# Optimization experiments

Measured on AMD Instinct MI355X. Metric: run time of the kernel, lower is better.

## Reference

```python
import jax, jax.numpy as jnp
import numpy as np

VOCAB, IMG_EMB, EMB, HID, P = 10000, 1024, 512, 512, 49
B, T = 64, 50


def setup_inputs() -> dict:
    key = jax.random.key(0)
    ks = jax.random.split(key, 16)
    def lin(k, fin, fout):
        k1, k2 = jax.random.split(k)
        s = 1.0 / np.sqrt(fin)
        return (jax.random.uniform(k1, (fin, fout), minval=-s, maxval=s),
                jax.random.uniform(k2, (fout,), minval=-s, maxval=s))
    Wv, bv = lin(ks[0], IMG_EMB, EMB)
    Wh, bh = lin(ks[1], EMB, HID)
    Wm, bm = lin(ks[2], EMB, HID)
    Wl, bl = lin(ks[3], 2 * EMB + HID, 5 * HID)  # LSTM fc on cat([w_t, vg, h])
    Wav, bav = lin(ks[4], HID, HID)
    Wah, bah = lin(ks[5], HID, HID)
    Was, bas = lin(ks[6], HID, HID)
    Waz, baz = lin(ks[7], HID, 1)
    Wp, bp = lin(ks[8], HID, VOCAB)
    emb = jax.random.normal(ks[9], (VOCAB, EMB)) * 0.02
    return {
        'v': jax.random.normal(ks[10], (B, P, IMG_EMB)),
        'w': jax.random.randint(ks[11], (B, T), 0, VOCAB),
        'lengths': jax.random.randint(ks[12], (B,), 0, T),
        'emb': emb,
        'Wv': Wv, 'bv': bv, 'Wh': Wh, 'bh': bh, 'Wm': Wm, 'bm': bm,
        'Wl': Wl, 'bl': bl,
        'Wav': Wav, 'bav': bav, 'Wah': Wah, 'bah': bah,
        'Was': Was, 'bas': bas, 'Waz': Waz, 'baz': baz,
        'Wp': Wp, 'bp': bp,
    }


def reference(v, w, lengths, emb, Wv, bv, Wh, bh, Wm, bm, Wl, bl,
              Wav, bav, Wah, bah, Was, bas, Waz, baz, Wp, bp):
    we = emb[w]                        # [B,T,E] word embeddings
    v = v @ Wv + bv                    # [B,P,E] projected visual features
    vg = v.mean(axis=1)                # [B,E] global visual feature
    h0 = vg @ Wh + bh                  # [B,H]
    m0 = vg @ Wm + bm                  # [B,H]
    pv = v @ Wav + bav                 # precompute attention proj of v [B,P,H]

    def step(carry, wt):
        h_, m_ = carry
        x = jnp.concatenate([wt, vg, h_], axis=-1)        # [B, 2E+H]
        i, f, o, g, m5 = jnp.split(x @ Wl + bl, 5, axis=-1)
        i = jax.nn.sigmoid(i)
        f = jax.nn.sigmoid(f)
        o = jax.nn.sigmoid(o)
        m = i * jnp.tanh(m5) + f * m_
        tm = jnp.tanh(m)
        h = o * tm
        s = g * tm                                        # sentinel gate
        # adaptive attention over P regions + sentinel h slot
        ph = (h @ Wah + bah)[:, None, :]                  # [B,1,H]
        ps = (s @ Was + bas)[:, None, :]                  # [B,1,H]
        z = jnp.tanh(jnp.concatenate([pv, ph], axis=1) + ps)  # [B,P+1,H]
        a = jax.nn.softmax(z @ Waz + baz, axis=1)         # [B,P+1,1]
        c = jnp.sum(a * jnp.concatenate([v, h[:, None, :]], axis=1), axis=1)
        p = jax.nn.softmax((c + h) @ Wp + bp, axis=-1)    # [B,V]
        return (h, m), p

    _, ps = jax.lax.scan(step, (h0, m0), jnp.swapaxes(we, 0, 1))
    ps = jnp.swapaxes(ps, 0, 1)                           # [B,T,V]
    mask = jnp.arange(ps.shape[1])[None, :] < lengths[:, None]
    return ps * mask[..., None].astype(ps.dtype)
```

## Files before the change

kernel.cpp:

```cpp
#include <hip/hip_runtime.h>
#include <hip/hip_bf16.h>
#include <cstdint>
#include <cstddef>

#define Bn 64
#define Tn 50
#define Pn 49
#define En 512
#define Hn 512
#define Vn 10000
#define IEn 1024
#define G5 2560

typedef __attribute__((ext_vector_type(8))) short bf16x8;
typedef __attribute__((ext_vector_type(4))) float f32x4;

__device__ __forceinline__ float sigm(float x)  { return 1.0f / (1.0f + __expf(-x)); }
__device__ __forceinline__ float tanh_f(float x){ return 1.0f - 2.0f / (1.0f + __expf(2.0f * x)); }

__device__ __forceinline__ unsigned short f2b(float f) {
    union { float f; unsigned int u; } c; c.f = f;
    unsigned int u = c.u;
    u += 0x7fffu + ((u >> 16) & 1u);
    return (unsigned short)(u >> 16);
}
__device__ __forceinline__ float b2f(unsigned short u) {
    union { unsigned int u; float f; } c; c.u = ((unsigned int)u) << 16;
    return c.f;
}

template<bool GATHER>
__global__ __launch_bounds__(256)
void gemm64(const float* __restrict__ A, int lda,
            const float* __restrict__ B,
            float* __restrict__ C,
            int M, int N, int K,
            const float* __restrict__ bias,
            const float* __restrict__ rowadd, int rowDiv, long rowStride,
            const int* __restrict__ gidx)
{
    const int n0 = blockIdx.x * 64;
    const int m0 = blockIdx.y * 64;
    const long koff = (long)blockIdx.z * K;
    const float* Bp = B + koff * N;
    float* Cp = C + (gridDim.z > 1 ? (size_t)blockIdx.z * (size_t)M * (size_t)N : (size_t)0);

    __shared__ float As[16][64];
    __shared__ float Bs[16][64];

    const int tid = threadIdx.x;
    const int tx = tid & 15;
    const int ty = tid >> 4;
    const int ra = tid >> 2;
    const int ca = (tid & 3) << 2;

    long arow = GATHER ? (long)gidx[m0 + ra] : (long)(m0 + ra);
    const float* Arow = A + arow * (long)lda + koff + ca;

    const int kl = ty;
    const int nb = tx << 2;
    const int ncol = n0 + nb;

    float acc[4][4] = {{0.f,0.f,0.f,0.f},{0.f,0.f,0.f,0.f},{0.f,0.f,0.f,0.f},{0.f,0.f,0.f,0.f}};

    for (int k0 = 0; k0 < K; k0 += 16) {
        float4 av = *(const float4*)(Arow + k0);
        float4 bv;
        const float* bptr = Bp + (long)(k0 + kl) * N + ncol;
        if (ncol + 3 < N) {
            bv = *(const float4*)bptr;
        } else {
            bv.x = (ncol + 0 < N) ? bptr[0] : 0.f;
            bv.y = (ncol + 1 < N) ? bptr[1] : 0.f;
            bv.z = (ncol + 2 < N) ? bptr[2] : 0.f;
            bv.w = (ncol + 3 < N) ? bptr[3] : 0.f;
        }
        __syncthreads();
        As[ca + 0][ra] = av.x; As[ca + 1][ra] = av.y;
        As[ca + 2][ra] = av.z; As[ca + 3][ra] = av.w;
        *(float4*)&Bs[kl][nb] = bv;
        __syncthreads();
        #pragma unroll
        for (int kk = 0; kk < 16; kk++) {
            const float4 a = *(const float4*)&As[kk][ty << 2];
            const float4 b = *(const float4*)&Bs[kk][tx << 2];
            const float a_[4] = {a.x, a.y, a.z, a.w};
            const float b_[4] = {b.x, b.y, b.z, b.w};
            #pragma unroll
            for (int i = 0; i < 4; i++)
                #pragma unroll
                for (int j = 0; j < 4; j++)
                    acc[i][j] = fmaf(a_[i], b_[j], acc[i][j]);
        }
    }

    #pragma unroll
    for (int i = 0; i < 4; i++) {
        const int rr = m0 + (ty << 2) + i;
        #pragma unroll
        for (int j = 0; j < 4; j++) {
            const int cc = n0 + (tx << 2) + j;
            if (cc < N) {
                float v = acc[i][j];
                if (bias)   v += bias[cc];
                if (rowadd) v += rowadd[(long)(rr / rowDiv) * rowStride + cc];
                Cp[(long)rr * N + cc] = v;
            }
        }
    }
}

template<int OUTF, int OUTB, int GM, int SWZ>
__global__ __launch_bounds__(256)
void gemm_mfma(const unsigned short* __restrict__ A,
               const unsigned short* __restrict__ BT,
               float* __restrict__ Cf, unsigned short* __restrict__ Cb,
               int M, int N, int K,
               const float* __restrict__ bias,
               const float* __restrict__ rowadd, int rowDiv,
               const int* __restrict__ ridx, const int* __restrict__ dcnt,
               int mtiles)
{
    __shared__ __align__(16) unsigned short Asm[128][40];
    __shared__ __align__(16) unsigned short Bsm[128][40];

    int Meff = M;
    if (GM) Meff = *dcnt;
    int m0, n0;
    if (SWZ) {
        const int nwg = gridDim.x;
        const int q = nwg >> 3, rm = nwg & 7;
        const int xcd = blockIdx.x & 7, pos = blockIdx.x >> 3;
        const int swz = (xcd < rm ? xcd * (q + 1) : rm * (q + 1) + (xcd - rm) * q) + pos;
        m0 = (swz % mtiles) * 128;
        n0 = (swz / mtiles) * 128;
    } else {
        n0 = blockIdx.x * 128;
        m0 = blockIdx.y * 128;
    }
    if (GM && m0 >= Meff) return;

    const int tid = threadIdx.x;
    const int lane = tid & 63;
    const int wid = tid >> 6;
    const int wm = wid >> 1;
    const int wn = wid & 1;

    const int r0 = tid >> 2;
    const int kg = tid & 3;

    const int ar0 = m0 + r0, ar1 = m0 + r0 + 64;
    const int br0 = n0 + r0, br1 = n0 + r0 + 64;
    long arow0, arow1;
    if (GM) {
        arow0 = (ar0 < Meff) ? (long)ridx[ar0] : 0;
        arow1 = (ar1 < Meff) ? (long)ridx[ar1] : 0;
    } else {
        arow0 = ar0; arow1 = ar1;
    }

    f32x4 acc[4][4] = {};
    const uint4 zero4 = {0u, 0u, 0u, 0u};

    uint4 a0, a1, b0, b1;
    {
        const long ka = (long)kg * 8;
        a0 = (GM || ar0 < Meff) ? *(const uint4*)(A + arow0 * K + ka) : zero4;
        a1 = (GM || ar1 < Meff) ? *(const uint4*)(A + arow1 * K + ka) : zero4;
        b0 = (br0 < N) ? *(const uint4*)(BT + (long)br0 * K + ka) : zero4;
        b1 = (br1 < N) ? *(const uint4*)(BT + (long)br1 * K + ka) : zero4;
    }

    for (int k0 = 0; k0 < K; k0 += 32) {
        __syncthreads();
        *(uint4*)&Asm[r0     ][kg * 8] = a0;
        *(uint4*)&Asm[r0 + 64][kg * 8] = a1;
        *(uint4*)&Bsm[r0     ][kg * 8] = b0;
        *(uint4*)&Bsm[r0 + 64][kg * 8] = b1;
        __syncthreads();

        if (k0 + 32 < K) {
            const long ka = (long)(k0 + 32) + kg * 8;
            a0 = (GM || ar0 < Meff) ? *(const uint4*)(A + arow0 * K + ka) : zero4;
            a1 = (GM || ar1 < Meff) ? *(const uint4*)(A + arow1 * K + ka) : zero4;
            b0 = (br0 < N) ? *(const uint4*)(BT + (long)br0 * K + ka) : zero4;
            b1 = (br1 < N) ? *(const uint4*)(BT + (long)br1 * K + ka) : zero4;
        }

        bf16x8 af[4], bfr[4];
        const int arow = wm * 64 + (lane & 15);
        const int brow = wn * 64 + (lane & 15);
        const int kcol = (lane >> 4) * 8;
        #pragma unroll
        for (int i = 0; i < 4; i++) {
            af[i]  = *(const bf16x8*)&Asm[arow + i * 16][kcol];
            bfr[i] = *(const bf16x8*)&Bsm[brow + i * 16][kcol];
        }
        #pragma unroll
        for (int mi = 0; mi < 4; mi++)
            #pragma unroll
            for (int ni = 0; ni < 4; ni++)
                acc[mi][ni] = __builtin_amdgcn_mfma_f32_16x16x32_bf16(af[mi], bfr[ni], acc[mi][ni], 0, 0, 0);
    }

    const int crow = m0 + wm * 64 + (lane >> 4) * 4;
    const int ccol0 = n0 + wn * 64 + (lane & 15);
    #pragma unroll
    for (int ni = 0; ni < 4; ni++) {
        const int col = ccol0 + ni * 16;
        if (col >= N) continue;
        const float bvv = bias ? bias[col] : 0.f;
        #pragma unroll
        for (int mi = 0; mi < 4; mi++) {
            #pragma unroll
            for (int r = 0; r < 4; r++) {
                const int rr = crow + mi * 16 + r;
                if (rr < Meff) {
                    const long orow = GM ? (long)ridx[rr] : (long)rr;
                    float v = acc[mi][ni][r] + bvv;
                    if (rowadd) v += rowadd[(long)(rr / rowDiv) * N + col];
                    if (OUTF) Cf[orow * N + col] = v;
                    if (OUTB) Cb[orow * N + col] = f2b(v);
                }
            }
        }
    }
}

__global__ __launch_bounds__(256)
void transpose_bf16(const float* __restrict__ in, unsigned short* __restrict__ out,
                    int K, int N, int istride)
{
    __shared__ float tile[32][33];
    const int k0 = blockIdx.y * 32;
    const int n0 = blockIdx.x * 32;
    const int tx = threadIdx.x & 31, ty = threadIdx.x >> 5;
    #pragma unroll
    for (int j = 0; j < 4; j++) {
        int k = k0 + ty + j * 8, n = n0 + tx;
        tile[ty + j * 8][tx] = (k < K && n < N) ? in[(long)k * istride + n] : 0.f;
    }
    __syncthreads();
    #pragma unroll
    for (int j = 0; j < 4; j++) {
        int n = n0 + ty + j * 8, k = k0 + tx;
        if (n < N && k < K) out[(long)n * K + k] = f2b(tile[tx][ty + j * 8]);
    }
}

__global__ __launch_bounds__(256)
void transpose2_G5(const float* __restrict__ Wl,
                   unsigned short* __restrict__ O0, unsigned short* __restrict__ O1)
{
    const float* in = Wl + (blockIdx.z ? (size_t)1024 * G5 : (size_t)0);
    unsigned short* out = blockIdx.z ? O1 : O0;
    __shared__ float tile[32][33];
    const int k0 = blockIdx.y * 32;
    const int n0 = blockIdx.x * 32;
    const int tx = threadIdx.x & 31, ty = threadIdx.x >> 5;
    #pragma unroll
    for (int j = 0; j < 4; j++)
        tile[ty + j * 8][tx] = in[(long)(k0 + ty + j * 8) * G5 + n0 + tx];
    __syncthreads();
    #pragma unroll
    for (int j = 0; j < 4; j++)
        out[(long)(n0 + ty + j * 8) * 512 + k0 + tx] = f2b(tile[tx][ty + j * 8]);
}

__global__ __launch_bounds__(256)
void transpose3_bf16(const float* __restrict__ A0, const float* __restrict__ A1,
                     const float* __restrict__ A2,
                     unsigned short* __restrict__ O0, unsigned short* __restrict__ O1,
                     unsigned short* __restrict__ O2)
{
    const float* in = (blockIdx.z == 0) ? A0 : (blockIdx.z == 1) ? A1 : A2;
    unsigned short* out = (blockIdx.z == 0) ? O0 : (blockIdx.z == 1) ? O1 : O2;
    __shared__ float tile[32][33];
    const int k0 = blockIdx.y * 32;
    const int n0 = blockIdx.x * 32;
    const int tx = threadIdx.x & 31, ty = threadIdx.x >> 5;
    #pragma unroll
    for (int j = 0; j < 4; j++)
        tile[ty + j * 8][tx] = in[(long)(k0 + ty + j * 8) * 512 + n0 + tx];
    __syncthreads();
    #pragma unroll
    for (int j = 0; j < 4; j++)
        out[(long)(n0 + ty + j * 8) * 512 + k0 + tx] = f2b(tile[tx][ty + j * 8]);
}

__global__ void convert_bf16(const float* __restrict__ in, unsigned short* __restrict__ out, int n4)
{
    int i = blockIdx.x * 256 + threadIdx.x;
    if (i < n4) {
        float4 v = ((const float4*)in)[i];
        ushort4 u;
        u.x = f2b(v.x); u.y = f2b(v.y); u.z = f2b(v.z); u.w = f2b(v.w);
        ((ushort4*)out)[i] = u;
    }
}

__global__ void gather_convert(const float* __restrict__ emb, const int* __restrict__ w,
                               unsigned short* __restrict__ out)
{
    const int r = blockIdx.x;
    const long row = w[r];
    const float4 v = ((const float4*)(emb + row * 512))[threadIdx.x];
    ushort4 u;
    u.x = f2b(v.x); u.y = f2b(v.y); u.z = f2b(v.z); u.w = f2b(v.w);
    ((ushort4*)(out + (long)r * 512))[threadIdx.x] = u;
}

__global__ void compact_rows(const int* __restrict__ len, int* __restrict__ ridx, int* __restrict__ dcnt)
{
    const int b = threadIdx.x;
    int L = len[b]; L = L < 0 ? 0 : (L > Tn ? Tn : L);
    int off = L;
    #pragma unroll
    for (int s = 1; s < 64; s <<= 1) {
        int n = __shfl_up(off, s);
        if (b >= s) off += n;
    }
    const int start = off - L;
    if (b == 63) *dcnt = off;
    for (int t = 0; t < L; t++) ridx[start + t] = b * Tn + t;
}

__global__ void vg_mean(const unsigned short* __restrict__ vproj, float* __restrict__ vg)
{
    const int tid = blockIdx.x * 256 + threadIdx.x;
    const int b = tid >> 9, e = tid & 511;
    const unsigned short* p = vproj + (long)b * Pn * En + e;
    float s = 0.f;
    #pragma unroll 7
    for (int q = 0; q < Pn; q++) s += b2f(p[q * En]);
    vg[tid] = s * (1.0f / 49.0f);
}

__global__ void h0m0(const float* __restrict__ vg,
                     const float* __restrict__ Wh, const float* __restrict__ bh,
                     const float* __restrict__ Wm, const float* __restrict__ bm,
                     unsigned short* __restrict__ h0b, float* __restrict__ m)
{
    __shared__ float vgs[512];
    const int b = blockIdx.x, e = threadIdx.x;
    vgs[e] = vg[b * 512 + e];
    __syncthreads();
    float a1 = bh[e], a2 = bm[e];
    #pragma unroll 8
    for (int k = 0; k < 512; k++) {
        const float x = vgs[k];
        a1 = fmaf(x, Wh[(long)k * 512 + e], a1);
        a2 = fmaf(x, Wm[(long)k * 512 + e], a2);
    }
    h0b[b * 512 + e] = f2b(a1);
    m[b * 512 + e] = a2;
}

__global__ __launch_bounds__(256)
void scan_step(int t, const float* __restrict__ base,
               const unsigned short* __restrict__ hcur,
               unsigned short* __restrict__ hnxt,
               float* __restrict__ mF,
               const unsigned short* __restrict__ W3T,
               float* __restrict__ HsF, unsigned short* __restrict__ Hsb,
               unsigned short* __restrict__ Ssb)
{
    __shared__ __align__(16) unsigned short Wh_s[5][8][520];

    const int tid = threadIdx.x;
    const int lane = tid & 63, wv = tid >> 6;
    const int e0 = blockIdx.x * 8;
    const int col = lane & 15;
    const int fk = (lane >> 4) * 8;
    const int bb = wv * 16 + (lane & 15);

    bf16x8 Ah[16];
    #pragma unroll
    for (int ch = 0; ch < 16; ch++)
        Ah[ch] = *(const bf16x8*)(hcur + (long)bb * 512 + ch * 32 + fk);

    for (int idx = tid; idx < 40 * 64; idx += 256) {
        const int row = idx >> 6, seg = idx & 63;
        const int g = row >> 3, c = row & 7;
        *(uint4*)&Wh_s[g][c][seg * 8] =
            *(const uint4*)(W3T + (long)(g * 512 + e0 + c) * 512 + seg * 8);
    }

    const int rbase = wv * 16 + (lane >> 4) * 4;
    const int ecol = e0 + (col & 7);
    float bse[5][4], mv[4];
    if (col < 8) {
        #pragma unroll
        for (int r = 0; r < 4; r++) {
            const long rrow = (long)(rbase + r) * Tn + t;
            const float* bp = base + rrow * G5 + ecol;
            bse[0][r] = bp[0];    bse[1][r] = bp[512];  bse[2][r] = bp[1024];
            bse[3][r] = bp[1536]; bse[4][r] = bp[2048];
            mv[r] = mF[(rbase + r) * 512 + ecol];
        }
    }

    __syncthreads();

    const unsigned short* B0 = &Wh_s[(col >> 3)    ][col & 7][0];
    const unsigned short* B1 = &Wh_s[2 + (col >> 3)][col & 7][0];
    const unsigned short* B2 = &Wh_s[4][col & 7][0];

    f32x4 a0 = {}, a1 = {}, a2 = {};
    #pragma unroll
    for (int ch = 0; ch < 16; ch++) {
        const int ko = ch * 32 + fk;
        a0 = __builtin_amdgcn_mfma_f32_16x16x32_bf16(Ah[ch], *(const bf16x8*)(B0 + ko), a0, 0, 0, 0);
        a1 = __builtin_amdgcn_mfma_f32_16x16x32_bf16(Ah[ch], *(const bf16x8*)(B1 + ko), a1, 0, 0, 0);
        a2 = __builtin_amdgcn_mfma_f32_16x16x32_bf16(Ah[ch], *(const bf16x8*)(B2 + ko), a2, 0, 0, 0);
    }

    #pragma unroll
    for (int r = 0; r < 4; r++) {
        const float fsh = __shfl_xor(a0[r], 8);
        const float gsh = __shfl_xor(a1[r], 8);
        if (col < 8) {
            const int b = rbase + r;
            const float gi = a0[r] + bse[0][r];
            const float gf = fsh   + bse[1][r];
            const float go = a1[r] + bse[2][r];
            const float gg = gsh   + bse[3][r];
            const float g5 = a2[r] + bse[4][r];
            const float iv = sigm(gi), fv = sigm(gf), ov = sigm(go);
            const float mn = fmaf(iv, tanh_f(g5), fv * mv[r]);
            const float tm = tanh_f(mn);
            const float hh = ov * tm, ss = gg * tm;
            const unsigned short hhi = f2b(hh);
            const long hoff = (long)b * 512 + ecol;
            const long rrow = (long)b * Tn + t;
            mF[hoff] = mn;
            hnxt[hoff] = hhi;
            HsF[rrow * 512 + ecol] = hh;
            Hsb[rrow * 512 + ecol] = hhi;
            Ssb[rrow * 512 + ecol] = f2b(ss);
        }
    }
}

__global__ __launch_bounds__(256)
void attn(const unsigned short* __restrict__ vproj, const float* __restrict__ pv,
          const float* __restrict__ PH, const float* __restrict__ PS,
          const float* __restrict__ Hs, const float* __restrict__ Waz,
          const float* __restrict__ baz, unsigned short* __restrict__ CHb,
          const int* __restrict__ len)
{
    const int r = (blockIdx.x & 7) * 400 + (blockIdx.x >> 3);
    const int b = r / Tn;
    if ((r % Tn) >= len[b]) return;
    const int tid = threadIdx.x;
    const int lane = tid & 63, wid = tid >> 6;

    __shared__ float ps_s[512];
    __shared__ float ph_s[512];
    __shared__ float alog[64];

    for (int i = tid; i < 512; i += 256) {
        ps_s[i] = PS[(long)r * 512 + i];
        ph_s[i] = PH[(long)r * 512 + i];
    }
    __syncthreads();

    const float4 wz0 = *(const float4*)(Waz + lane * 8);
    const float4 wz1 = *(const float4*)(Waz + lane * 8 + 4);
    const float4 q0  = *(const float4*)&ps_s[lane * 8];
    const float4 q1  = *(const float4*)&ps_s[lane * 8 + 4];

    for (int slot = wid; slot < Pn + 1; slot += 4) {
        const float* src = (slot < Pn) ? (pv + ((long)b * Pn + slot) * 512)
                                       : (const float*)ph_s;
        const float4 x0 = *(const float4*)(src + lane * 8);
        const float4 x1 = *(const float4*)(src + lane * 8 + 4);
        float d = 0.f;
        d = fmaf(tanh_f(x0.x + q0.x), wz0.x, d);
        d = fmaf(tanh_f(x0.y + q0.y), wz0.y, d);
        d = fmaf(tanh_f(x0.z + q0.z), wz0.z, d);
        d = fmaf(tanh_f(x0.w + q0.w), wz0.w, d);
        d = fmaf(tanh_f(x1.x + q1.x), wz1.x, d);
        d = fmaf(tanh_f(x1.y + q1.y), wz1.y, d);
        d = fmaf(tanh_f(x1.z + q1.z), wz1.z, d);
        d = fmaf(tanh_f(x1.w + q1.w), wz1.w, d);
        #pragma unroll
        for (int s = 32; s >= 1; s >>= 1) d += __shfl_xor(d, s);
        if (lane == 0) alog[slot] = d + baz[0];
    }
    __syncthreads();

    if (wid == 0) {
        const float v = (lane < Pn + 1) ? alog[lane] : -3.4e38f;
        float mx = v;
        #pragma unroll
        for (int s = 32; s >= 1; s >>= 1) mx = fmaxf(mx, __shfl_xor(mx, s));
        const float ev = (lane < Pn + 1) ? __expf(v - mx) : 0.f;
        float sm = ev;
        #pragma unroll
        for (int s = 32; s >= 1; s >>= 1) sm += __shfl_xor(sm, s);
        if (lane < Pn + 1) alog[lane] = ev / sm;
    }
    __syncthreads();

    const float a49 = alog[Pn];
    for (int ee = tid; ee < 512; ee += 256) {
        const float hval = Hs[(long)r * 512 + ee];
        float c = a49 * hval;
        const unsigned short* vp = vproj + (long)b * Pn * 512 + ee;
        #pragma unroll 7
        for (int q = 0; q < Pn; q++) c = fmaf(alog[q], b2f(vp[q * 512]), c);
        CHb[(long)r * 512 + ee] = f2b(c + hval);
    }
}

__global__ __launch_bounds__(256)
void softmax_mask(float* __restrict__ out, const int* __restrict__ lengths)
{
    const int r = blockIdx.x, b = r / Tn, t = r % Tn;
    float* row = out + (long)r * Vn;
    const int tid = threadIdx.x;
    float4* row4 = (float4*)row;

    if (t >= lengths[b]) {
        f32x4* rowv = (f32x4*)row;
        const f32x4 z = {0.f, 0.f, 0.f, 0.f};
        for (int i = tid; i < Vn / 4; i += 256)
            __builtin_nontemporal_store(z, &rowv[i]);
        return;
    }

    __shared__ float red[4];
    const int lane = tid & 63, wid = tid >> 6;

    float4 rv[10];
    float mx = -3.4e38f;
    #pragma unroll
    for (int j = 0; j < 10; j++) {
        const int i = tid + j * 256;
        if (i < Vn / 4) {
            rv[j] = row4[i];
            mx = fmaxf(mx, fmaxf(fmaxf(rv[j].x, rv[j].y), fmaxf(rv[j].z, rv[j].w)));
        }
    }
    #pragma unroll
    for (int s = 32; s >= 1; s >>= 1) mx = fmaxf(mx, __shfl_xor(mx, s));
    if (lane == 0) red[wid] = mx;
    __syncthreads();
    mx = fmaxf(fmaxf(red[0], red[1]), fmaxf(red[2], red[3]));
    __syncthreads();

    float sm = 0.f;
    #pragma unroll
    for (int j = 0; j < 10; j++) {
        const int i = tid + j * 256;
        if (i < Vn / 4) {
            rv[j].x = __expf(rv[j].x - mx);
            rv[j].y = __expf(rv[j].y - mx);
            rv[j].z = __expf(rv[j].z - mx);
            rv[j].w = __expf(rv[j].w - mx);
            sm += rv[j].x + rv[j].y + rv[j].z + rv[j].w;
        }
    }
    #pragma unroll
    for (int s = 32; s >= 1; s >>= 1) sm += __shfl_xor(sm, s);
    if (lane == 0) red[wid] = sm;
    __syncthreads();
    sm = red[0] + red[1] + red[2] + red[3];
    const float inv = 1.0f / sm;

    #pragma unroll
    for (int j = 0; j < 10; j++) {
        const int i = tid + j * 256;
        if (i < Vn / 4) {
            rv[j].x *= inv; rv[j].y *= inv; rv[j].z *= inv; rv[j].w *= inv;
            row4[i] = rv[j];
        }
    }
}

extern "C" void kernel_launch(void* const* d_in, const int* in_sizes, int n_in,
                              void* d_out, int out_size, void* d_ws, size_t ws_size,
                              hipStream_t stream)
{
    (void)in_sizes; (void)n_in; (void)out_size; (void)ws_size;
    const float* v   = (const float*)d_in[0];
    const int*   w   = (const int*)  d_in[1];
    const int*   len = (const int*)  d_in[2];
    const float* emb = (const float*)d_in[3];
    const float* Wv  = (const float*)d_in[4];
    const float* bv  = (const float*)d_in[5];
    const float* Wh  = (const float*)d_in[6];
    const float* bh  = (const float*)d_in[7];
    const float* Wm  = (const float*)d_in[8];
    const float* bm  = (const float*)d_in[9];
    const float* Wl  = (const float*)d_in[10];
    const float* bl  = (const float*)d_in[11];
    const float* Wav = (const float*)d_in[12];
    const float* bav = (const float*)d_in[13];
    const float* Wah = (const float*)d_in[14];
    const float* bah = (const float*)d_in[15];
    const float* Was = (const float*)d_in[16];
    const float* bas = (const float*)d_in[17];
    const float* Waz = (const float*)d_in[18];
    const float* baz = (const float*)d_in[19];
    const float* Wp  = (const float*)d_in[20];
    const float* bp  = (const float*)d_in[21];
    float* out_f = (float*)d_out;

    char* wsp = (char*)d_ws;
    size_t off = 0;
    auto walloc = [&](size_t bytes) -> void* {
        void* r = wsp + off;
        off += (bytes + 255) & ~(size_t)255;
        return r;
    };
    unsigned short* WpT    = (unsigned short*)walloc((size_t)Vn * 512 * 2);
    unsigned short* WvT    = (unsigned short*)walloc((size_t)512 * 1024 * 2);
    unsigned short* WlT0   = (unsigned short*)walloc((size_t)G5 * 512 * 2);
    unsigned short* WavT   = (unsigned short*)walloc((size_t)512 * 512 * 2);
    unsigned short* WahT   = (unsigned short*)walloc((size_t)512 * 512 * 2);
    unsigned short* WasT   = (unsigned short*)walloc((size_t)512 * 512 * 2);
    unsigned short* vprojb = (unsigned short*)walloc((size_t)3136 * 512 * 2);
    unsigned short* CHb    = (unsigned short*)walloc((size_t)3200 * 512 * 2);
    float* vg   = (float*)walloc((size_t)64 * 512 * 4);
    unsigned short* hB = (unsigned short*)walloc((size_t)2 * 64 * 512 * 2);
    float* mbuf = (float*)walloc((size_t)64 * 512 * 4);
    float* vgw  = (float*)walloc((size_t)64 * G5 * 4);
    int*   ridx = (int*)walloc((size_t)3200 * 4);
    int*   dcnt = (int*)walloc(256);

    char* sp = (char*)(out_f + (size_t)3200 * G5);
    size_t off2 = 0;
    auto salloc = [&](size_t bytes) -> void* {
        void* r = sp + off2;
        off2 += (bytes + 255) & ~(size_t)255;
        return r;
    };
    unsigned short* vB  = (unsigned short*)salloc((size_t)3136 * 1024 * 2);
    unsigned short* WEb = (unsigned short*)salloc((size_t)3200 * 512 * 2);
    float* pvb = (float*)salloc((size_t)3136 * 512 * 4);
    float* HsF = (float*)salloc((size_t)3200 * 512 * 4);
    unsigned short* Hsb = (unsigned short*)salloc((size_t)3200 * 512 * 2);
    unsigned short* Ssb = (unsigned short*)salloc((size_t)3200 * 512 * 2);
    float* PHb = (float*)salloc((size_t)3200 * 512 * 4);
    float* PSb = (float*)salloc((size_t)3200 * 512 * 4);
    unsigned short* W3T = (unsigned short*)salloc((size_t)G5 * 512 * 2);

    transpose_bf16<<<dim3(512/32, 1024/32), 256, 0, stream>>>(Wv, WvT, 1024, 512, 512);
    transpose2_G5<<<dim3(G5/32, 16, 2), 256, 0, stream>>>(Wl, WlT0, W3T);
    transpose3_bf16<<<dim3(16, 16, 3), 256, 0, stream>>>(Wav, Wah, Was, WavT, WahT, WasT);
    transpose_bf16<<<dim3((Vn + 31)/32, 16), 256, 0, stream>>>(Wp, WpT, 512, Vn, Vn);
    convert_bf16<<<(3136*1024/4 + 255)/256, 256, 0, stream>>>(v, vB, 3136*1024/4);
    gather_convert<<<3200, 128, 0, stream>>>(emb, w, WEb);
    compact_rows<<<1, 64, 0, stream>>>(len, ridx, dcnt);

    gemm_mfma<0,1,0,0><<<dim3(4, 25), 256, 0, stream>>>(vB, WvT, nullptr, vprojb,
                                                        3136, 512, 1024, bv, nullptr, 1,
                                                        nullptr, nullptr, 0);
    vg_mean<<<128, 256, 0, stream>>>(vprojb, vg);
    h0m0<<<64, 512, 0, stream>>>(vg, Wh, bh, Wm, bm, hB, mbuf);
    gemm64<false><<<dim3(40, 1, 1), 256, 0, stream>>>(vg, 512, Wl + (size_t)512 * G5, vgw,
                                                      64, G5, 512, bl, nullptr, 1, 0, nullptr);
    gemm_mfma<1,0,0,0><<<dim3(4, 25), 256, 0, stream>>>(vprojb, WavT, pvb, nullptr,
                                                        3136, 512, 512, bav, nullptr, 1,
                                                        nullptr, nullptr, 0);
    gemm_mfma<1,0,0,1><<<500, 256, 0, stream>>>(WEb, WlT0, out_f, nullptr,
                                                3200, G5, 512, nullptr, vgw, Tn,
                                                nullptr, nullptr, 25);
    for (int t = 0; t < Tn; t++) {
        const size_t cur = (size_t)(t & 1) * (64 * 512);
        const size_t nxt = (size_t)((t + 1) & 1) * (64 * 512);
        scan_step<<<64, 256, 0, stream>>>(t, out_f, hB + cur, hB + nxt, mbuf, W3T,
                                          HsF, Hsb, Ssb);
    }
    gemm_mfma<1,0,1,0><<<dim3(4, 25), 256, 0, stream>>>(Hsb, WahT, PHb, nullptr,
                                                        3200, 512, 512, bah, nullptr, 1,
                                                        ridx, dcnt, 0);
    gemm_mfma<1,0,1,0><<<dim3(4, 25), 256, 0, stream>>>(Ssb, WasT, PSb, nullptr,
                                                        3200, 512, 512, bas, nullptr, 1,
                                                        ridx, dcnt, 0);
    attn<<<3200, 256, 0, stream>>>(vprojb, pvb, PHb, PSb, HsF, Waz, baz, CHb, len);
    gemm_mfma<1,0,1,1><<<1975, 256, 0, stream>>>(CHb, WpT, out_f, nullptr,
                                                 3200, Vn, 512, bp, nullptr, 1,
                                                 ridx, dcnt, 25);
    softmax_mask<<<3200, 256, 0, stream>>>(out_f, len);
}
```

Baseline: 802.5 us.

## Fuse attention projections into scan steps, compact LSTM input GEMM, add wide output GEMM

Removes the two separate Wah/Was projection GEMMs. Each scan step now also computes the previous step's h·Wah and s·Was from the h it already holds in registers, with one extra step launched at the end. The word-embedding LSTM input GEMM now computes only the valid (compacted) rows, and its rowadd indexing uses the real output row. The vocabulary projection uses a new 128x256-tile GEMM to cut the number of workgroups and reuse A tiles more. The trade-offs are one extra scan launch, more shared memory per scan block, and higher register pressure in the wide GEMM.

```diff
diff --git a/kernel.cpp b/kernel.cpp
--- a/kernel.cpp
+++ b/kernel.cpp
@@ -218,9 +218,109 @@
                 if (rr < Meff) {
                     const long orow = GM ? (long)ridx[rr] : (long)rr;
                     float v = acc[mi][ni][r] + bvv;
-                    if (rowadd) v += rowadd[(long)(rr / rowDiv) * N + col];
+                    if (rowadd) v += rowadd[(orow / rowDiv) * N + col];
                     if (OUTF) Cf[orow * N + col] = v;
                     if (OUTB) Cb[orow * N + col] = f2b(v);
+                }
+            }
+        }
+    }
+}
+
+__global__ __launch_bounds__(256)
+void gemm_n256(const unsigned short* __restrict__ A,
+               const unsigned short* __restrict__ BT,
+               float* __restrict__ Cf,
+               int N, int K,
+               const float* __restrict__ bias,
+               const int* __restrict__ ridx, const int* __restrict__ dcnt,
+               int mtiles)
+{
+    __shared__ __align__(16) unsigned short Asm[128][40];
+    __shared__ __align__(16) unsigned short Bsm[256][40];
+
+    const int Meff = *dcnt;
+    int m0, n0;
+    {
+        const int nwg = gridDim.x;
+        const int q = nwg >> 3, rm = nwg & 7;
+        const int xcd = blockIdx.x & 7, pos = blockIdx.x >> 3;
+        const int swz = (xcd < rm ? xcd * (q + 1) : rm * (q + 1) + (xcd - rm) * q) + pos;
+        m0 = (swz % mtiles) * 128;
+        n0 = (swz / mtiles) * 256;
+    }
+    if (m0 >= Meff) return;
+
+    const int tid = threadIdx.x;
+    const int lane = tid & 63;
+    const int wid = tid >> 6;
+    const int wm = wid >> 1;
+    const int wn = wid & 1;
+    const int r0 = tid >> 2;
+    const int kg = tid & 3;
+
+    const int ar0 = m0 + r0, ar1 = m0 + r0 + 64;
+    const long arow0 = (ar0 < Meff) ? (long)ridx[ar0] : 0;
+    const long arow1 = (ar1 < Meff) ? (long)ridx[ar1] : 0;
+
+    f32x4 acc[4][8] = {};
+    const uint4 zero4 = {0u, 0u, 0u, 0u};
+
+    uint4 aR0, aR1, bR[4];
+    auto load = [&](int k0) {
+        const long ka = (long)k0 + kg * 8;
+        aR0 = *(const uint4*)(A + arow0 * K + ka);
+        aR1 = *(const uint4*)(A + arow1 * K + ka);
+        #pragma unroll
+        for (int j = 0; j < 4; j++) {
+            const int br = n0 + r0 + j * 64;
+            bR[j] = (br < N) ? *(const uint4*)(BT + (long)br * K + ka) : zero4;
+        }
+    };
+    load(0);
+
+    const int arowf = wm * 64 + (lane & 15);
+    const int browf = wn * 128 + (lane & 15);
+    const int kcol = (lane >> 4) * 8;
+
+    for (int k0 = 0; k0 < K; k0 += 32) {
+        __syncthreads();
+        *(uint4*)&Asm[r0     ][kg * 8] = aR0;
+        *(uint4*)&Asm[r0 + 64][kg * 8] = aR1;
+        #pragma unroll
+        for (int j = 0; j < 4; j++)
+            *(uint4*)&Bsm[r0 + j * 64][kg * 8] = bR[j];
+        __syncthreads();
+
+        if (k0 + 32 < K) load(k0 + 32);
+
+        bf16x8 af[4], bfr[8];
+        #pragma unroll
+        for (int i = 0; i < 4; i++) af[i] = *(const bf16x8*)&Asm[arowf + i * 16][kcol];
+        #pragma unroll
+        for (int i = 0; i < 8; i++) bfr[i] = *(const bf16x8*)&Bsm[browf + i * 16][kcol];
+        #pragma unroll
+        for (int mi = 0; mi < 4; mi++)
+            #pragma unroll
+            for (int ni = 0; ni < 8; ni++)
+                acc[mi][ni] = __builtin_amdgcn_mfma_f32_16x16x32_bf16(af[mi], bfr[ni], acc[mi][ni], 0, 0, 0);
+    }
+
+    const int crow = m0 + wm * 64 + (lane >> 4) * 4;
+    const int ccol0 = n0 + wn * 128 + (lane & 15);
+    #pragma unroll
+    for (int ni = 0; ni < 8; ni++) {
+        const int col = ccol0 + ni * 16;
+        if (col >= N) continue;
+        const float bvv = bias[col];
+        #pragma unroll
+        for (int mi = 0; mi < 4; mi++) {
+            #pragma unroll
+            for (int r = 0; r < 4; r++) {
+                const int rr = crow + mi * 16 + r;
+                if (rr < Meff) {
+                    const long orow = (long)ridx[rr];
+                    Cf[orow * N + col] = acc[mi][ni][r] + bvv;
                 }
             }
         }
@@ -362,10 +462,15 @@
                unsigned short* __restrict__ hnxt,
                float* __restrict__ mF,
                const unsigned short* __restrict__ W3T,
+               const unsigned short* __restrict__ WahT,
+               const unsigned short* __restrict__ WasT,
+               const float* __restrict__ bah, const float* __restrict__ bas,
                float* __restrict__ HsF, unsigned short* __restrict__ Hsb,
-               unsigned short* __restrict__ Ssb)
+               unsigned short* __restrict__ Ssb,
+               float* __restrict__ PHb, float* __restrict__ PSb)
 {
     __shared__ __align__(16) unsigned short Wh_s[5][8][520];
+    __shared__ __align__(16) unsigned short B3_s[16][520];
 
     const int tid = threadIdx.x;
     const int lane = tid & 63, wv = tid >> 6;
@@ -385,11 +490,18 @@
         *(uint4*)&Wh_s[g][c][seg * 8] =
             *(const uint4*)(W3T + (long)(g * 512 + e0 + c) * 512 + seg * 8);
     }
+    for (int idx = tid; idx < 16 * 64; idx += 256) {
+        const int row = idx >> 6, seg = idx & 63;
+        const unsigned short* src = (row < 8)
+            ? WahT + (long)(e0 + row) * 512
+            : WasT + (long)(e0 + row - 8) * 512;
+        *(uint4*)&B3_s[row][seg * 8] = *(const uint4*)(src + seg * 8);
+    }
 
     const int rbase = wv * 16 + (lane >> 4) * 4;
     const int ecol = e0 + (col & 7);
     float bse[5][4], mv[4];
-    if (col < 8) {
+    if (t < Tn && col < 8) {
         #pragma unroll
         for (int r = 0; r < 4; r++) {
             const long rrow = (long)(rbase + r) * Tn + t;
@@ -402,42 +514,57 @@
 
     __syncthreads();
 
-    const unsigned short* B0 = &Wh_s[(col >> 3)    ][col & 7][0];
-    const unsigned short* B1 = &Wh_s[2 + (col >> 3)][col & 7][0];
-    const unsigned short* B2 = &Wh_s[4][col & 7][0];
-
-    f32x4 a0 = {}, a1 = {}, a2 = {};
-    #pragma unroll
-    for (int ch = 0; ch < 16; ch++) {
-        const int ko = ch * 32 + fk;
-        a0 = __builtin_amdgcn_mfma_f32_16x16x32_bf16(Ah[ch], *(const bf16x8*)(B0 + ko), a0, 0, 0, 0);
-        a1 = __builtin_amdgcn_mfma_f32_16x16x32_bf16(Ah[ch], *(const bf16x8*)(B1 + ko), a1, 0, 0, 0);
-        a2 = __builtin_amdgcn_mfma_f32_16x16x32_bf16(Ah[ch], *(const bf16x8*)(B2 + ko), a2, 0, 0, 0);
-    }
-
-    #pragma unroll
-    for (int r = 0; r < 4; r++) {
-        const float fsh = __shfl_xor(a0[r], 8);
-        const float gsh = __shfl_xor(a1[r], 8);
-        if (col < 8) {
-            const int b = rbase + r;
-            const float gi = a0[r] + bse[0][r];
-            const float gf = fsh   + bse[1][r];
-            const float go = a1[r] + bse[2][r];
-            const float gg = gsh   + bse[3][r];
-            const float g5 = a2[r] + bse[4][r];
-            const float iv = sigm(gi), fv = sigm(gf), ov = sigm(go);
-            const float mn = fmaf(iv, tanh_f(g5), fv * mv[r]);
-            const float tm = tanh_f(mn);
-            const float hh = ov * tm, ss = gg * tm;
-            const unsigned short hhi = f2b(hh);
-            const long hoff = (long)b * 512 + ecol;
-            const long rrow = (long)b * Tn + t;
-            mF[hoff] = mn;
-            hnxt[hoff] = hhi;
-            HsF[rrow * 512 + ecol] = hh;
-            Hsb[rrow * 512 + ecol] = hhi;
-            Ssb[rrow * 512 + ecol] = f2b(ss);
+    if (t > 0) {
+        const unsigned short* B3p = &B3_s[col][0];
+        f32x4 a3 = {};
+        #pragma unroll
+        for (int ch = 0; ch < 16; ch++)
+            a3 = __builtin_amdgcn_mfma_f32_16x16x32_bf16(Ah[ch], *(const bf16x8*)(B3p + ch * 32 + fk), a3, 0, 0, 0);
+        const float pb = (col < 8) ? bah[ecol] : bas[ecol];
+        float* dst = (col < 8) ? PHb : PSb;
+        #pragma unroll
+        for (int r = 0; r < 4; r++)
+            dst[((long)(rbase + r) * Tn + (t - 1)) * 512 + ecol] = a3[r] + pb;
+    }
+
+    if (t < Tn) {
+        const unsigned short* B0 = &Wh_s[(col >> 3)    ][col & 7][0];
+        const unsigned short* B1 = &Wh_s[2 + (col >> 3)][col & 7][0];
+        const unsigned short* B2 = &Wh_s[4][col & 7][0];
+
+        f32x4 a0 = {}, a1 = {}, a2 = {};
+        #pragma unroll
+        for (int ch = 0; ch < 16; ch++) {
+            const int ko = ch * 32 + fk;
+            a0 = __builtin_amdgcn_mfma_f32_16x16x32_bf16(Ah[ch], *(const bf16x8*)(B0 + ko), a0, 0, 0, 0);
+            a1 = __builtin_amdgcn_mfma_f32_16x16x32_bf16(Ah[ch], *(const bf16x8*)(B1 + ko), a1, 0, 0, 0);
+            a2 = __builtin_amdgcn_mfma_f32_16x16x32_bf16(Ah[ch], *(const bf16x8*)(B2 + ko), a2, 0, 0, 0);
+        }
+
+        #pragma unroll
+        for (int r = 0; r < 4; r++) {
+            const float fsh = __shfl_xor(a0[r], 8);
+            const float gsh = __shfl_xor(a1[r], 8);
+            if (col < 8) {
+                const int b = rbase + r;
+                const float gi = a0[r] + bse[0][r];
+                const float gf = fsh   + bse[1][r];
+                const float go = a1[r] + bse[2][r];
+                const float gg = gsh   + bse[3][r];
+                const float g5 = a2[r] + bse[4][r];
+                const float iv = sigm(gi), fv = sigm(gf), ov = sigm(go);
+                const float mn = fmaf(iv, tanh_f(g5), fv * mv[r]);
+                const float tm = tanh_f(mn);
+                const float hh = ov * tm, ss = gg * tm;
+                const unsigned short hhi = f2b(hh);
+                const long hoff = (long)b * 512 + ecol;
+                const long rrow = (long)b * Tn + t;
+                mF[hoff] = mn;
+                hnxt[hoff] = hhi;
+                HsF[rrow * 512 + ecol] = hh;
+                Hsb[rrow * 512 + ecol] = hhi;
+                Ssb[rrow * 512 + ecol] = f2b(ss);
+            }
         }
     }
 }
@@ -665,24 +792,17 @@
     gemm_mfma<1,0,0,0><<<dim3(4, 25), 256, 0, stream>>>(vprojb, WavT, pvb, nullptr,
                                                         3136, 512, 512, bav, nullptr, 1,
                                                         nullptr, nullptr, 0);
-    gemm_mfma<1,0,0,1><<<500, 256, 0, stream>>>(WEb, WlT0, out_f, nullptr,
+    gemm_mfma<1,0,1,1><<<500, 256, 0, stream>>>(WEb, WlT0, out_f, nullptr,
                                                 3200, G5, 512, nullptr, vgw, Tn,
-                                                nullptr, nullptr, 25);
-    for (int t = 0; t < Tn; t++) {
+                                                ridx, dcnt, 25);
+    for (int t = 0; t <= Tn; t++) {
         const size_t cur = (size_t)(t & 1) * (64 * 512);
         const size_t nxt = (size_t)((t + 1) & 1) * (64 * 512);
         scan_step<<<64, 256, 0, stream>>>(t, out_f, hB + cur, hB + nxt, mbuf, W3T,
-                                          HsF, Hsb, Ssb);
-    }
-    gemm_mfma<1,0,1,0><<<dim3(4, 25), 256, 0, stream>>>(Hsb, WahT, PHb, nullptr,
-                                                        3200, 512, 512, bah, nullptr, 1,
-                                                        ridx, dcnt, 0);
-    gemm_mfma<1,0,1,0><<<dim3(4, 25), 256, 0, stream>>>(Ssb, WasT, PSb, nullptr,
-                                                        3200, 512, 512, bas, nullptr, 1,
-                                                        ridx, dcnt, 0);
+                                          WahT, WasT, bah, bas,
+                                          HsF, Hsb, Ssb, PHb, PSb);
+    }
     attn<<<3200, 256, 0, stream>>>(vprojb, pvb, PHb, PSb, HsF, Waz, baz, CHb, len);
-    gemm_mfma<1,0,1,1><<<1975, 256, 0, stream>>>(CHb, WpT, out_f, nullptr,
-                                                 3200, Vn, 512, bp, nullptr, 1,
-                                                 ridx, dcnt, 25);
+    gemm_n256<<<1000, 256, 0, stream>>>(CHb, WpT, out_f, Vn, 512, bp, ridx, dcnt, 25);
     softmax_mask<<<3200, 256, 0, stream>>>(out_f, len);
 }
```

Result: slower. 857.3 us (+6.8%).
